# Kernel tuning notes

Measured on AMD Instinct MI355X. Metric: run time of the kernel, lower is better.

## Reference

```python
import jax, jax.numpy as jnp
import numpy as np

B = 16      # batch (num jagged sequences)
N = 1024    # max seq length (mask size n)
D = 512     # embedding_dim
H = 8       # num_heads
DA = 64     # attention_dim per head
DV = 64     # linear_hidden_dim per head
EPS = 1e-6


def setup_inputs() -> dict:
    key = jax.random.key(0)
    k0, k1, k2, k3 = jax.random.split(key, 4)
    lengths = 512 + 16 * np.arange(B)            # deterministic jagged lengths, all <= N
    offsets = np.concatenate([[0], np.cumsum(lengths)]).astype(np.int64)  # (B+1,)
    T = int(offsets[-1])                          # 10112 total tokens
    x = jax.random.normal(k0, (T, D), jnp.float32)
    uvqk = jax.random.normal(k1, (D, 2 * H * DV + 2 * H * DA), jnp.float32) * 0.02
    # torch Linear weight is (out_features, in_features) = (D, H*DV), xavier-uniform scale
    lim = float(np.sqrt(6.0 / (D + H * DV)))
    o_weight = jax.random.uniform(k2, (D, H * DV), jnp.float32, -lim, lim)
    o_bias = jax.random.uniform(k3, (D,), jnp.float32, -0.01, 0.01)
    invalid_attn_mask = jnp.tril(jnp.ones((N, N), jnp.float32))  # causal {0,1} mask
    return {
        "x": x,
        "x_offsets": jnp.asarray(offsets),
        "invalid_attn_mask": invalid_attn_mask,
        "uvqk": uvqk,
        "o_weight": o_weight,
        "o_bias": o_bias,
    }


def _layer_norm(x):
    # F.layer_norm over last dim, no elementwise affine
    m = jnp.mean(x, axis=-1, keepdims=True)
    v = jnp.mean(jnp.square(x - m), axis=-1, keepdims=True)
    return (x - m) / jnp.sqrt(v + EPS)


def _jagged_to_padded(values, offsets, n):
    # values: (T, C) -> (B, n, C), zero padded
    lengths = offsets[1:] - offsets[:-1]               # (B,)
    pos = jnp.arange(n)                                # (n,)
    idx = offsets[:-1, None] + pos[None, :]            # (B, n)
    valid = pos[None, :] < lengths[:, None]            # (B, n)
    idx = jnp.where(valid, idx, 0)
    return values[idx] * valid[..., None].astype(values.dtype)


def _dense_to_jagged(padded, offsets, T):
    # padded: (B, n, C) -> (T, C)
    tok = jnp.arange(T)
    b = jnp.searchsorted(offsets, tok, side="right") - 1   # batch id per token
    p = tok - offsets[b]                                   # position within sequence
    return padded[b, p]


def reference(x, x_offsets, invalid_attn_mask, uvqk, o_weight, o_bias):
    T = x.shape[0]
    n = invalid_attn_mask.shape[-1]
    normed_x = _layer_norm(x)                              # (T, D)
    mm = jax.nn.silu(normed_x @ uvqk)                      # (T, 2*H*DV + 2*H*DA)
    u, v, q, k = jnp.split(mm, [H * DV, 2 * H * DV, 2 * H * DV + H * DA], axis=1)
    pq = _jagged_to_padded(q, x_offsets, n).reshape(-1, n, H, DA)  # (B,n,H,DA)
    pk = _jagged_to_padded(k, x_offsets, n).reshape(-1, n, H, DA)
    pv = _jagged_to_padded(v, x_offsets, n).reshape(-1, n, H, DV)
    qk = jnp.einsum("bqhd,bkhd->bhqk", pq, pk)             # (B,H,n,n)
    qk = (jax.nn.silu(qk) / n) * invalid_attn_mask[None, None]
    attn = jnp.einsum("bhqk,bkhd->bqhd", qk, pv).reshape(-1, n, H * DV)
    attn_j = _dense_to_jagged(attn, x_offsets, T)          # (T, H*DV)
    o_input = u * _layer_norm(attn_j)
    return o_input @ o_weight.T + o_bias + x
```

## Files before the change

kernel.cpp:

```cpp
#include <hip/hip_runtime.h>
#include <hip/hip_bf16.h>
#include <math.h>

typedef short bf16x8 __attribute__((ext_vector_type(8)));
typedef float f32x4 __attribute__((ext_vector_type(4)));

#define MFMA16x16(a, b, c) __builtin_amdgcn_mfma_f32_16x16x32_bf16(a, b, c, 0, 0, 0)

__device__ __forceinline__ float silu_f(float v) { return v / (1.0f + __expf(-v)); }
__device__ __forceinline__ int swz128(int b) { return b ^ (((b >> 7) & 7) << 4); }

__device__ __forceinline__ unsigned short f2bf(float f) {
  union { float f; unsigned u; } x; x.f = f;
  unsigned r = x.u + 0x7fffu + ((x.u >> 16) & 1u);
  return (unsigned short)(r >> 16);
}
__device__ __forceinline__ float bf2f(unsigned short h) {
  union { unsigned u; float f; } x; x.u = ((unsigned)h) << 16;
  return x.f;
}

__device__ __forceinline__ void gload_lds16(const void* g, void* l) {
  __builtin_amdgcn_global_load_lds((__attribute__((address_space(1))) unsigned int*)g,
                                   (__attribute__((address_space(3))) unsigned int*)l,
                                   16, 0, 0);
}

__global__ void k_prep(const int* __restrict__ raw, int Bp1, int* __restrict__ offs,
                       int* __restrict__ tiles, int qtmax) {
  __shared__ int s_off[128], s_nt[128], s_cnt[128], s_base[128];
  int t = threadIdx.x;
  int B = Bp1 - 1;
  bool is64 = (raw[3] == 0);
  if (t < Bp1) { int v = is64 ? raw[2 * t] : raw[t]; offs[t] = v; s_off[t] = v; }
  __syncthreads();
  if (t < B) s_nt[t] = (s_off[t + 1] - s_off[t] + 31) >> 5;
  __syncthreads();
  if (t < qtmax) {
    int c = 0;
    for (int b = 0; b < B; ++b) c += (t < s_nt[b]) ? 1 : 0;
    s_cnt[t] = c;
  }
  __syncthreads();
  if (t < qtmax) {
    int basev = 0;
    for (int q2 = t + 1; q2 < qtmax; ++q2) basev += s_cnt[q2];
    s_base[t] = basev;
  }
  __syncthreads();
  if (t == 0) tiles[0] = (s_base[0] + s_cnt[0]) * 8;
  for (int i = t; i < qtmax * B; i += 256) {
    int qt = i / B, b = i - qt * B;
    if (qt < s_nt[b]) {
      int rank = 0;
      for (int b2 = 0; b2 < b; ++b2) rank += (qt < s_nt[b2]) ? 1 : 0;
      tiles[1 + s_base[qt] + rank] = (b << 16) | qt;
    }
  }
}

__global__ __launch_bounds__(256) void k_conv_uvqkT(const float* __restrict__ uvqk,
                                                    unsigned short* __restrict__ uvqkT) {
  __shared__ float tile[32][33];
  int n0 = blockIdx.x * 32, k0 = blockIdx.y * 32;
  int tx = threadIdx.x & 31;
  int ty = threadIdx.x >> 5;
#pragma unroll
  for (int i = 0; i < 4; ++i)
    tile[ty + 8 * i][tx] = uvqk[(size_t)(k0 + ty + 8 * i) * 2048 + n0 + tx];
  __syncthreads();
#pragma unroll
  for (int i = 0; i < 4; ++i) {
    int nn = ty + 8 * i;
    uvqkT[(size_t)(n0 + nn) * 512 + k0 + tx] = f2bf(tile[tx][nn]);
  }
}

__global__ __launch_bounds__(256) void k_conv_bf16(const float* __restrict__ in,
                                                   unsigned short* __restrict__ out, int n) {
  int i = blockIdx.x * 256 + threadIdx.x;
  if (i < n) out[i] = f2bf(in[i]);
}

__global__ __launch_bounds__(256) void k_ln_x(const float* __restrict__ x,
                                              unsigned short* __restrict__ normed, int T) {
  int lane = threadIdx.x & 63, wid = threadIdx.x >> 6;
  int row = blockIdx.x * 4 + wid;
  if (row >= T) return;
  const float4* xr = (const float4*)(x + (size_t)row * 512);
  float4 a = xr[lane * 2], b = xr[lane * 2 + 1];
  float s = a.x + a.y + a.z + a.w + b.x + b.y + b.z + b.w;
  float s2 = a.x * a.x + a.y * a.y + a.z * a.z + a.w * a.w +
             b.x * b.x + b.y * b.y + b.z * b.z + b.w * b.w;
#pragma unroll
  for (int m = 1; m < 64; m <<= 1) { s += __shfl_xor(s, m); s2 += __shfl_xor(s2, m); }
  float mean = s * (1.0f / 512.0f);
  float var = s2 * (1.0f / 512.0f) - mean * mean;
  float rstd = rsqrtf(var + 1e-6f);
  float v[8] = {a.x, a.y, a.z, a.w, b.x, b.y, b.z, b.w};
  unsigned short o[8];
#pragma unroll
  for (int j = 0; j < 8; ++j) o[j] = f2bf((v[j] - mean) * rstd);
  *(uint4*)(normed + (size_t)row * 512 + lane * 8) = *(uint4*)o;
}

__global__ __launch_bounds__(256) void k_ln_mul_u(const unsigned short* __restrict__ attnb,
                                                  const unsigned short* __restrict__ mm,
                                                  unsigned short* __restrict__ oin, int T) {
  int lane = threadIdx.x & 63, wid = threadIdx.x >> 6;
  int row = blockIdx.x * 4 + wid;
  if (row >= T) return;
  uint4 av = *(const uint4*)(attnb + (size_t)row * 512 + lane * 8);
  const unsigned short* ae = (const unsigned short*)&av;
  float v[8];
#pragma unroll
  for (int j = 0; j < 8; ++j) v[j] = bf2f(ae[j]);
  float s = 0.f, s2 = 0.f;
#pragma unroll
  for (int j = 0; j < 8; ++j) { s += v[j]; s2 += v[j] * v[j]; }
#pragma unroll
  for (int m = 1; m < 64; m <<= 1) { s += __shfl_xor(s, m); s2 += __shfl_xor(s2, m); }
  float mean = s * (1.0f / 512.0f);
  float var = s2 * (1.0f / 512.0f) - mean * mean;
  float rstd = rsqrtf(var + 1e-6f);
  uint4 ub = *(const uint4*)(mm + (size_t)row * 2048 + lane * 8);
  const unsigned short* us = (const unsigned short*)&ub;
  unsigned short o[8];
#pragma unroll
  for (int j = 0; j < 8; ++j) o[j] = f2bf((v[j] - mean) * rstd * bf2f(us[j]));
  *(uint4*)(oin + (size_t)row * 512 + lane * 8) = *(uint4*)o;
}

template <int MODE>
__global__ __launch_bounds__(256) void k_gemm_bt(const unsigned short* __restrict__ A,
                                                 const unsigned short* __restrict__ Bt,
                                                 void* __restrict__ Cout,
                                                 const float* __restrict__ bias,
                                                 const float* __restrict__ xres,
                                                 int M, int Nn, int K, int ntn) {
  __shared__ __align__(16) char lds[32768];
  char* ldsA = lds;
  char* ldsB = lds + 16384;
  int bid = blockIdx.x;
  int mt = bid / ntn, nt = bid - mt * ntn;
  int m0 = mt * 128, n0 = nt * 128;
  int tid = threadIdx.x, lane = tid & 63, wid = tid >> 6;
  int wm = wid >> 1, wn = wid & 1;
  int fr = lane & 15, fq = lane >> 4;
  f32x4 acc[4][4] = {};
  int nK = K >> 6;
  int lco = (lane & 7) * 16;
  int lrow8 = lane >> 3;
  for (int kt = 0; kt < nK; ++kt) {
    int k0 = kt << 6;
#pragma unroll
    for (int p = 0; p < 4; ++p) {
      int chunk = wid * 4 + p;
      int row = chunk * 8 + lrow8;
      int colb = lco ^ ((row & 7) << 4);
      int ar = m0 + row; if (ar >= M) ar = M - 1;
      gload_lds16((const char*)(A + (size_t)ar * K + k0) + colb, ldsA + chunk * 1024);
      gload_lds16((const char*)(Bt + (size_t)(n0 + row) * K + k0) + colb, ldsB + chunk * 1024);
    }
    __syncthreads();
    bf16x8 af[4][2], bfr[4][2];
#pragma unroll
    for (int mi = 0; mi < 4; ++mi) {
      int r = wm * 64 + mi * 16 + fr;
#pragma unroll
      for (int kk = 0; kk < 2; ++kk)
        af[mi][kk] = *(const bf16x8*)(ldsA + swz128(r * 128 + kk * 64 + fq * 16));
    }
#pragma unroll
    for (int ni = 0; ni < 4; ++ni) {
      int r = wn * 64 + ni * 16 + fr;
#pragma unroll
      for (int kk = 0; kk < 2; ++kk)
        bfr[ni][kk] = *(const bf16x8*)(ldsB + swz128(r * 128 + kk * 64 + fq * 16));
    }
#pragma unroll
    for (int mi = 0; mi < 4; ++mi)
#pragma unroll
      for (int ni = 0; ni < 4; ++ni) {
        acc[mi][ni] = MFMA16x16(af[mi][0], bfr[ni][0], acc[mi][ni]);
        acc[mi][ni] = MFMA16x16(af[mi][1], bfr[ni][1], acc[mi][ni]);
      }
    __syncthreads();
  }
#pragma unroll
  for (int mi = 0; mi < 4; ++mi) {
#pragma unroll
    for (int j = 0; j < 4; ++j) {
      int r = m0 + wm * 64 + mi * 16 + fq * 4 + j;
      if (r >= M) continue;
#pragma unroll
      for (int ni = 0; ni < 4; ++ni) {
        int c = n0 + wn * 64 + ni * 16 + fr;
        float v = acc[mi][ni][j];
        if (MODE == 0) {
          ((unsigned short*)Cout)[(size_t)r * Nn + c] = f2bf(silu_f(v));
        } else {
          ((float*)Cout)[(size_t)r * Nn + c] = v + bias[c] + xres[(size_t)r * 512 + c];
        }
      }
    }
  }
}

__global__ __launch_bounds__(256) void k_kv(const unsigned short* __restrict__ mm,
                                            const int* __restrict__ offs,
                                            unsigned short* __restrict__ kC,
                                            unsigned short* __restrict__ vT, int ns) {
  int bh = blockIdx.x; int b = bh >> 3, h = bh & 7;
  int off = offs[b], len = offs[b + 1] - offs[b];
  int tid = threadIdx.x;
  int npad = (len + 63) & ~63;
  const unsigned short* kp = mm + (size_t)off * 2048 + 1536 + h * 64;
  unsigned short* kc = kC + (size_t)bh * ns * 64;
  for (int i = tid; i < npad * 8; i += 256) {
    int row = i >> 3, c8 = (i & 7) * 8;
    uint4 v = {0u, 0u, 0u, 0u};
    if (row < len) v = *(const uint4*)(kp + (size_t)row * 2048 + c8);
    *(uint4*)(kc + row * 64 + c8) = v;
  }
  int lane = tid & 63, w = tid >> 6;
  const unsigned short* vp = mm + (size_t)off * 2048 + 512 + h * 64 + lane;
  unsigned short* vt = vT + ((size_t)bh * 64 + lane) * ns;
  for (int c = w; c < (npad >> 3); c += 4) {
    int s8 = c << 3;
    unsigned short r[8];
#pragma unroll
    for (int j = 0; j < 8; ++j)
      r[j] = (s8 + j < len) ? vp[(size_t)(s8 + j) * 2048] : (unsigned short)0;
    *(uint4*)(vt + s8) = *(uint4*)r;
  }
}

__global__ __launch_bounds__(256) void k_attn3(const unsigned short* __restrict__ mm,
                                               const unsigned short* __restrict__ kC,
                                               const unsigned short* __restrict__ vT,
                                               const int* __restrict__ offs,
                                               const int* __restrict__ tiles,
                                               unsigned short* __restrict__ attnb,
                                               float inv_n, int ns) {
  __shared__ __align__(16) char sP[16384];
  int tid = threadIdx.x, lane = tid & 63, wid = tid >> 6;
  int w = blockIdx.x * 4 + wid;
  if (w >= tiles[0]) return;
  int e = tiles[1 + (w >> 3)];
  int h = w & 7;
  int b = e >> 16, qt = e & 0xffff;
  int bh = b * 8 + h;
  int off = offs[b], len = offs[b + 1] - offs[b];
  int qb = qt * 32;
  int fr = lane & 15, fq = lane >> 4;
  const unsigned short* qp = mm + (size_t)off * 2048 + 1024 + h * 64;
  const unsigned short* kcp = kC + (size_t)bh * ns * 64;
  const unsigned short* vtp = vT + (size_t)bh * 64 * ns;
  bf16x8 aq[2][2];
#pragma unroll
  for (int mi = 0; mi < 2; ++mi) {
    int qr = qb + mi * 16 + fr; if (qr >= len) qr = len - 1;
#pragma unroll
    for (int kk = 0; kk < 2; ++kk)
      aq[mi][kk] = *(const bf16x8*)(qp + (size_t)qr * 2048 + kk * 32 + fq * 8);
  }
  f32x4 accO[2][4] = {};
  char* pw = sP + wid * 4096;
  int nkt = (qb >> 6) + 1;
  for (int kt = 0; kt < nkt; ++kt) {
    int s0 = kt << 6;
    f32x4 sacc[2][4] = {};
#pragma unroll
    for (int ni = 0; ni < 4; ++ni) {
      const unsigned short* kr = kcp + (size_t)(s0 + ni * 16 + fr) * 64 + fq * 8;
      bf16x8 k0 = *(const bf16x8*)kr;
      bf16x8 k1 = *(const bf16x8*)(kr + 32);
#pragma unroll
      for (int mi = 0; mi < 2; ++mi) {
        sacc[mi][ni] = MFMA16x16(aq[mi][0], k0, sacc[mi][ni]);
        sacc[mi][ni] = MFMA16x16(aq[mi][1], k1, sacc[mi][ni]);
      }
    }
    bf16x8 vf[4][2];
#pragma unroll
    for (int nd = 0; nd < 4; ++nd)
#pragma unroll
      for (int kk = 0; kk < 2; ++kk)
        vf[nd][kk] = *(const bf16x8*)(vtp + (size_t)(nd * 16 + fr) * ns + s0 + kk * 32 + fq * 8);
#pragma unroll
    for (int mi = 0; mi < 2; ++mi)
#pragma unroll
      for (int ni = 0; ni < 4; ++ni)
#pragma unroll
        for (int j = 0; j < 4; ++j) {
          int pq = qb + mi * 16 + fq * 4 + j;
          int ps = s0 + ni * 16 + fr;
          float v = (ps <= pq) ? silu_f(sacc[mi][ni][j]) * inv_n : 0.0f;
          *(unsigned short*)(pw + swz128((mi * 16 + fq * 4 + j) * 128 + (ni * 16 + fr) * 2)) =
              f2bf(v);
        }
    bf16x8 pa[2][2];
#pragma unroll
    for (int mi = 0; mi < 2; ++mi) {
      pa[mi][0] = *(const bf16x8*)(pw + swz128((mi * 16 + fr) * 128 + fq * 16));
      pa[mi][1] = *(const bf16x8*)(pw + swz128((mi * 16 + fr) * 128 + 64 + fq * 16));
    }
#pragma unroll
    for (int nd = 0; nd < 4; ++nd)
#pragma unroll
      for (int mi = 0; mi < 2; ++mi) {
        accO[mi][nd] = MFMA16x16(pa[mi][0], vf[nd][0], accO[mi][nd]);
        accO[mi][nd] = MFMA16x16(pa[mi][1], vf[nd][1], accO[mi][nd]);
      }
  }
#pragma unroll
  for (int mi = 0; mi < 2; ++mi)
#pragma unroll
    for (int nd = 0; nd < 4; ++nd)
#pragma unroll
      for (int j = 0; j < 4; ++j) {
        int pq = qb + mi * 16 + fq * 4 + j;
        if (pq < len)
          attnb[(size_t)(off + pq) * 512 + h * 64 + nd * 16 + fr] = f2bf(accO[mi][nd][j]);
      }
}

extern "C" void kernel_launch(void* const* d_in, const int* in_sizes, int n_in,
                              void* d_out, int out_size, void* d_ws, size_t ws_size,
                              hipStream_t stream) {
  const float* x = (const float*)d_in[0];
  const int* xoff = (const int*)d_in[1];
  const float* uvqk = (const float*)d_in[3];
  const float* ow = (const float*)d_in[4];
  const float* obias = (const float*)d_in[5];

  const int D = 512;
  int T = in_sizes[0] / D;
  int B = in_sizes[1] - 1;
  int nm = 1;
  while ((long long)nm * nm < (long long)in_sizes[2]) nm <<= 1;
  int qtmax = nm / 32;

  char* w = (char*)d_ws;
  size_t p = 0;
  auto alloc = [&](size_t bytes) { size_t r = p; p += (bytes + 255) & ~(size_t)255; return r; };
  int* offs = (int*)(w + alloc(sizeof(int) * (size_t)(B + 1)));
  int* tiles = (int*)(w + alloc(sizeof(int) * (size_t)(1 + B * qtmax)));
  unsigned short* normed = (unsigned short*)(w + alloc((size_t)T * 512 * 2));
  unsigned short* mm = (unsigned short*)(w + alloc((size_t)T * 2048 * 2));
  unsigned short* attnb = (unsigned short*)(w + alloc((size_t)T * 512 * 2));
  unsigned short* oin = (unsigned short*)(w + alloc((size_t)T * 512 * 2));
  unsigned short* uvqkT = (unsigned short*)(w + alloc((size_t)2048 * 512 * 2));
  unsigned short* owb = (unsigned short*)(w + alloc((size_t)512 * 512 * 2));
  unsigned short* vT = (unsigned short*)(w + alloc((size_t)B * 8 * 64 * (size_t)nm * 2));
  unsigned short* kC = (unsigned short*)(w + alloc((size_t)B * 8 * (size_t)nm * 64 * 2));

  k_prep<<<1, 256, 0, stream>>>(xoff, B + 1, offs, tiles, qtmax);
  k_conv_uvqkT<<<dim3(64, 16), 256, 0, stream>>>(uvqk, uvqkT);
  k_conv_bf16<<<1024, 256, 0, stream>>>(ow, owb, 512 * 512);
  k_ln_x<<<(T + 3) / 4, 256, 0, stream>>>(x, normed, T);
  int ntm = (T + 127) / 128;
  k_gemm_bt<0><<<ntm * 16, 256, 0, stream>>>(normed, uvqkT, (void*)mm, nullptr, nullptr,
                                             T, 2048, 512, 16);
  k_kv<<<B * 8, 256, 0, stream>>>(mm, offs, kC, vT, nm);
  int maxw = B * qtmax * 8;
  k_attn3<<<(maxw + 3) / 4, 256, 0, stream>>>(mm, kC, vT, offs, tiles, attnb,
                                              1.0f / (float)nm, nm);
  k_ln_mul_u<<<(T + 3) / 4, 256, 0, stream>>>(attnb, mm, oin, T);
  k_gemm_bt<1><<<ntm * 4, 256, 0, stream>>>(oin, owb, d_out, obias, x, T, 512, 512, 4);
}
```

Before: 223.6 us.

## Replace uvqk projection GEMM with 256x256 8-wave ping-pong pipelined kernel

Swaps the 128x128 tile GEMM for the input projection (T x 2048 x 512) with a new 512-thread kernel using 256x256 tiles, double-buffered LDS (128KB), and global->LDS loads split into quarters interleaved with four MFMA phases per K step, with explicit vmcnt waits, raw barriers and s_setprio. The aim is to hide global load latency behind MFMA work and raise per-block data reuse. The cost is heavy LDS use (one block per CU at most, despite launch_bounds asking for 2), many barriers per iteration, and fewer blocks (40x8=320 tiles) for a fairly small GEMM. The epilogue writes scalar bf16 values with silu applied.

Measured after the change: 232.0 us. 1.04x slower.

```diff
diff --git a/kernel.cpp b/kernel.cpp
--- a/kernel.cpp
+++ b/kernel.cpp
@@ -6,6 +6,12 @@
 typedef float f32x4 __attribute__((ext_vector_type(4)));
 
 #define MFMA16x16(a, b, c) __builtin_amdgcn_mfma_f32_16x16x32_bf16(a, b, c, 0, 0, 0)
+#define VMCNT(n) asm volatile("s_waitcnt vmcnt(" #n ")" ::: "memory")
+#define CFENCE asm volatile("" ::: "memory")
+
+__device__ __forceinline__ void barrier_raw() {
+  CFENCE; __builtin_amdgcn_s_barrier(); CFENCE;
+}
 
 __device__ __forceinline__ float silu_f(float v) { return v / (1.0f + __expf(-v)); }
 __device__ __forceinline__ int swz128(int b) { return b ^ (((b >> 7) & 7) << 4); }
@@ -129,6 +135,133 @@
 #pragma unroll
   for (int j = 0; j < 8; ++j) o[j] = f2bf((v[j] - mean) * rstd * bf2f(us[j]));
   *(uint4*)(oin + (size_t)row * 512 + lane * 8) = *(uint4*)o;
+}
+
+__global__ __launch_bounds__(512, 2) void k_gemm8p_silu(
+    const unsigned short* __restrict__ A, const unsigned short* __restrict__ Bt,
+    unsigned short* __restrict__ Cout, int M, int Nn, int K, int ntn) {
+  __shared__ __align__(16) char lds[131072];
+  int bid = blockIdx.x;
+  int mt = bid / ntn, nt = bid - mt * ntn;
+  int m0 = mt * 256, n0 = nt * 256;
+  int tid = threadIdx.x, lane = tid & 63, wid = tid >> 6;
+  int wm = wid >> 2, wn = wid & 3;
+  int fr = lane & 15, fq = lane >> 4;
+  f32x4 acc[8][4] = {};
+  int nK = K >> 6;
+
+  char* const ldsA = lds;
+  char* const ldsB = lds + 65536;
+  int srow = tid >> 3;
+  int scb = ((tid & 7) << 4) ^ ((srow & 7) << 4);
+  int sdst = wid * 1024 + lane * 16;
+
+  auto stageA = [&](char* buf, int kt2, int u) {
+    int row = u * 64 + srow;
+    int ar = m0 + row; if (ar >= M) ar = M - 1;
+    gload_lds16((const char*)(A + (size_t)ar * K + (kt2 << 6)) + scb,
+                buf + u * 8192 + sdst);
+  };
+  auto stageB = [&](char* buf, int kt2, int u) {
+    int row = u * 64 + srow;
+    gload_lds16((const char*)(Bt + (size_t)(n0 + row) * K + (kt2 << 6)) + scb,
+                buf + u * 8192 + sdst);
+  };
+  auto rdA = [&](const char* buf, int mi, int kk) -> bf16x8 {
+    int r = wm * 128 + mi * 16 + fr;
+    return *(const bf16x8*)(buf + swz128(r * 128 + kk * 64 + fq * 16));
+  };
+  auto rdB = [&](const char* buf, int ni, int kk) -> bf16x8 {
+    int r = wn * 64 + ni * 16 + fr;
+    return *(const bf16x8*)(buf + swz128(r * 128 + kk * 64 + fq * 16));
+  };
+
+#pragma unroll
+  for (int u = 0; u < 4; ++u) stageA(ldsA, 0, u);
+#pragma unroll
+  for (int u = 0; u < 4; ++u) stageB(ldsB, 0, u);
+  VMCNT(0);
+  barrier_raw();
+
+  int cur = 0;
+  for (int t = 0; t < nK; ++t) {
+    char* cA = ldsA + cur * 32768;
+    char* cB = ldsB + cur * 32768;
+    char* nA = ldsA + (cur ^ 1) * 32768;
+    char* nB = ldsB + (cur ^ 1) * 32768;
+    bool pf = (t + 1) < nK;
+    bf16x8 a[4][2], b[4][2];
+#pragma unroll
+    for (int mi = 0; mi < 4; ++mi) { a[mi][0] = rdA(cA, mi, 0); a[mi][1] = rdA(cA, mi, 1); }
+#pragma unroll
+    for (int ni = 0; ni < 2; ++ni) { b[ni][0] = rdB(cB, ni, 0); b[ni][1] = rdB(cB, ni, 1); }
+    if (pf) { stageA(nA, t + 1, 0); stageA(nA, t + 1, 2); }
+    barrier_raw();
+    __builtin_amdgcn_s_setprio(1);
+#pragma unroll
+    for (int mi = 0; mi < 4; ++mi)
+#pragma unroll
+      for (int ni = 0; ni < 2; ++ni) {
+        acc[mi][ni] = MFMA16x16(a[mi][0], b[ni][0], acc[mi][ni]);
+        acc[mi][ni] = MFMA16x16(a[mi][1], b[ni][1], acc[mi][ni]);
+      }
+    __builtin_amdgcn_s_setprio(0);
+    barrier_raw();
+#pragma unroll
+    for (int ni = 2; ni < 4; ++ni) { b[ni][0] = rdB(cB, ni, 0); b[ni][1] = rdB(cB, ni, 1); }
+    if (pf) { stageB(nB, t + 1, 0); stageB(nB, t + 1, 1); VMCNT(4); } else { VMCNT(0); }
+    barrier_raw();
+    __builtin_amdgcn_s_setprio(1);
+#pragma unroll
+    for (int mi = 0; mi < 4; ++mi)
+#pragma unroll
+      for (int ni = 2; ni < 4; ++ni) {
+        acc[mi][ni] = MFMA16x16(a[mi][0], b[ni][0], acc[mi][ni]);
+        acc[mi][ni] = MFMA16x16(a[mi][1], b[ni][1], acc[mi][ni]);
+      }
+    __builtin_amdgcn_s_setprio(0);
+    barrier_raw();
+#pragma unroll
+    for (int mi = 0; mi < 4; ++mi) { a[mi][0] = rdA(cA, mi + 4, 0); a[mi][1] = rdA(cA, mi + 4, 1); }
+    if (pf) { stageB(nB, t + 1, 2); stageB(nB, t + 1, 3); }
+    barrier_raw();
+    __builtin_amdgcn_s_setprio(1);
+#pragma unroll
+    for (int mi = 0; mi < 4; ++mi)
+#pragma unroll
+      for (int ni = 0; ni < 2; ++ni) {
+        acc[mi + 4][ni] = MFMA16x16(a[mi][0], b[ni][0], acc[mi + 4][ni]);
+        acc[mi + 4][ni] = MFMA16x16(a[mi][1], b[ni][1], acc[mi + 4][ni]);
+      }
+    __builtin_amdgcn_s_setprio(0);
+    barrier_raw();
+    if (pf) { stageA(nA, t + 1, 1); stageA(nA, t + 1, 3); VMCNT(2); }
+    barrier_raw();
+    __builtin_amdgcn_s_setprio(1);
+#pragma unroll
+    for (int mi = 0; mi < 4; ++mi)
+#pragma unroll
+      for (int ni = 2; ni < 4; ++ni) {
+        acc[mi + 4][ni] = MFMA16x16(a[mi][0], b[ni][0], acc[mi + 4][ni]);
+        acc[mi + 4][ni] = MFMA16x16(a[mi][1], b[ni][1], acc[mi + 4][ni]);
+      }
+    __builtin_amdgcn_s_setprio(0);
+    barrier_raw();
+    cur ^= 1;
+  }
+#pragma unroll
+  for (int mi = 0; mi < 8; ++mi) {
+#pragma unroll
+    for (int j = 0; j < 4; ++j) {
+      int r = m0 + wm * 128 + mi * 16 + fq * 4 + j;
+      if (r >= M) continue;
+#pragma unroll
+      for (int ni = 0; ni < 4; ++ni) {
+        int c = n0 + wn * 64 + ni * 16 + fr;
+        Cout[(size_t)r * Nn + c] = f2bf(silu_f(acc[mi][ni][j]));
+      }
+    }
+  }
 }
 
 template <int MODE>
@@ -360,13 +493,13 @@
   k_conv_uvqkT<<<dim3(64, 16), 256, 0, stream>>>(uvqk, uvqkT);
   k_conv_bf16<<<1024, 256, 0, stream>>>(ow, owb, 512 * 512);
   k_ln_x<<<(T + 3) / 4, 256, 0, stream>>>(x, normed, T);
-  int ntm = (T + 127) / 128;
-  k_gemm_bt<0><<<ntm * 16, 256, 0, stream>>>(normed, uvqkT, (void*)mm, nullptr, nullptr,
-                                             T, 2048, 512, 16);
+  int ntm8 = (T + 255) / 256;
+  k_gemm8p_silu<<<ntm8 * 8, 512, 0, stream>>>(normed, uvqkT, mm, T, 2048, 512, 8);
   k_kv<<<B * 8, 256, 0, stream>>>(mm, offs, kC, vT, nm);
   int maxw = B * qtmax * 8;
   k_attn3<<<(maxw + 3) / 4, 256, 0, stream>>>(mm, kC, vT, offs, tiles, attnb,
                                               1.0f / (float)nm, nm);
   k_ln_mul_u<<<(T + 3) / 4, 256, 0, stream>>>(attnb, mm, oin, T);
+  int ntm = (T + 127) / 128;
   k_gemm_bt<1><<<ntm * 4, 256, 0, stream>>>(oin, owb, d_out, obias, x, T, 512, 512, 4);
 }
```

## Fuse per-head Q/K/V scatter into UVQK GEMM epilogue and use 8-wave GEMM tiles

Applied to the files above, without the earlier changes.

The UVQK GEMM epilogue now writes u, per-head Q and K (row-major padded) and transposed V directly, using a per-token batch/position table built in the prep kernel. This removes the separate k_kv repack pass and the full T x 2048 intermediate buffer. A small zero-fill kernel covers the padded tails. The GEMM also moves to 512 threads with 8 waves each computing a 64x32 sub-tile, and every wave issues its own global-to-LDS loads. The cost is scattered 2-byte stores in the epilogue (V transposed stores are strided), which may hurt write coalescing.

Measured after the change: 233.4 us. +4.4%, slower.

```diff
diff --git a/kernel.cpp b/kernel.cpp
--- a/kernel.cpp
+++ b/kernel.cpp
@@ -27,7 +27,7 @@
 }
 
 __global__ void k_prep(const int* __restrict__ raw, int Bp1, int* __restrict__ offs,
-                       int* __restrict__ tiles, int qtmax) {
+                       int* __restrict__ tiles, int qtmax, int* __restrict__ tok2bp, int T) {
   __shared__ int s_off[128], s_nt[128], s_cnt[128], s_base[128];
   int t = threadIdx.x;
   int B = Bp1 - 1;
@@ -56,6 +56,32 @@
       for (int b2 = 0; b2 < b; ++b2) rank += (qt < s_nt[b2]) ? 1 : 0;
       tiles[1 + s_base[qt] + rank] = (b << 16) | qt;
     }
+  }
+  for (int i = t; i < T; i += 256) {
+    int b = 0;
+    for (int j = 0; j < B; ++j) b += (s_off[j + 1] <= i) ? 1 : 0;
+    tok2bp[i] = (b << 16) | (i - s_off[b]);
+  }
+}
+
+__global__ __launch_bounds__(256) void k_zfill(const int* __restrict__ offs,
+                                               unsigned short* __restrict__ kC,
+                                               unsigned short* __restrict__ vT, int ns) {
+  int bh = blockIdx.x, b = bh >> 3;
+  int len = offs[b + 1] - offs[b];
+  int npad = (len + 63) & ~63;
+  int tail = npad - len;
+  if (tail == 0) return;
+  int tid = threadIdx.x;
+  unsigned short* kc = kC + (size_t)bh * ns * 64 + (size_t)len * 64;
+  for (int i = tid; i < tail * 8; i += 256) {
+    uint4 z = {0u, 0u, 0u, 0u};
+    *(uint4*)(kc + i * 8) = z;
+  }
+  unsigned short* vt = vT + (size_t)bh * 64 * ns;
+  for (int i = tid; i < 64 * tail; i += 256) {
+    int d = i / tail, c = len + (i - d * tail);
+    vt[(size_t)d * ns + c] = 0;
   }
 }
 
@@ -105,7 +131,7 @@
 }
 
 __global__ __launch_bounds__(256) void k_ln_mul_u(const unsigned short* __restrict__ attnb,
-                                                  const unsigned short* __restrict__ mm,
+                                                  const unsigned short* __restrict__ mmu,
                                                   unsigned short* __restrict__ oin, int T) {
   int lane = threadIdx.x & 63, wid = threadIdx.x >> 6;
   int row = blockIdx.x * 4 + wid;
@@ -123,7 +149,7 @@
   float mean = s * (1.0f / 512.0f);
   float var = s2 * (1.0f / 512.0f) - mean * mean;
   float rstd = rsqrtf(var + 1e-6f);
-  uint4 ub = *(const uint4*)(mm + (size_t)row * 2048 + lane * 8);
+  uint4 ub = *(const uint4*)(mmu + (size_t)row * 512 + lane * 8);
   const unsigned short* us = (const unsigned short*)&ub;
   unsigned short o[8];
 #pragma unroll
@@ -132,111 +158,101 @@
 }
 
 template <int MODE>
-__global__ __launch_bounds__(256) void k_gemm_bt(const unsigned short* __restrict__ A,
-                                                 const unsigned short* __restrict__ Bt,
-                                                 void* __restrict__ Cout,
-                                                 const float* __restrict__ bias,
-                                                 const float* __restrict__ xres,
-                                                 int M, int Nn, int K, int ntn) {
+__global__ __launch_bounds__(512, 4) void k_gemm8w(
+    const unsigned short* __restrict__ A, const unsigned short* __restrict__ Bt,
+    int M, int K, int Nn, int ntn,
+    unsigned short* __restrict__ mmu, unsigned short* __restrict__ qC,
+    unsigned short* __restrict__ kC, unsigned short* __restrict__ vT,
+    const int* __restrict__ tok2bp, int ns,
+    float* __restrict__ Cout, const float* __restrict__ bias, const float* __restrict__ xres) {
   __shared__ __align__(16) char lds[32768];
-  char* ldsA = lds;
-  char* ldsB = lds + 16384;
+  char* const ldsA = lds;
+  char* const ldsB = lds + 16384;
   int bid = blockIdx.x;
   int mt = bid / ntn, nt = bid - mt * ntn;
   int m0 = mt * 128, n0 = nt * 128;
   int tid = threadIdx.x, lane = tid & 63, wid = tid >> 6;
-  int wm = wid >> 1, wn = wid & 1;
+  int wm = wid >> 2, wn = wid & 3;
   int fr = lane & 15, fq = lane >> 4;
-  f32x4 acc[4][4] = {};
+  f32x4 acc[4][2] = {};
   int nK = K >> 6;
-  int lco = (lane & 7) * 16;
-  int lrow8 = lane >> 3;
+  int srow = wid * 16 + (lane >> 3);
+  int scb = (((lane & 7) ^ (lane >> 3)) << 4);
+  char* const dstA0 = ldsA + wid * 2048;
+  char* const dstA1 = ldsA + wid * 2048 + 1024;
+  char* const dstB0 = ldsB + wid * 2048;
+  char* const dstB1 = ldsB + wid * 2048 + 1024;
+  int ar0 = m0 + srow; if (ar0 >= M) ar0 = M - 1;
+  int ar1 = m0 + srow + 8; if (ar1 >= M) ar1 = M - 1;
+  const char* gA0 = (const char*)(A + (size_t)ar0 * K) + scb;
+  const char* gA1 = (const char*)(A + (size_t)ar1 * K) + scb;
+  const char* gB0 = (const char*)(Bt + (size_t)(n0 + srow) * K) + scb;
+  const char* gB1 = (const char*)(Bt + (size_t)(n0 + srow + 8) * K) + scb;
+
   for (int kt = 0; kt < nK; ++kt) {
-    int k0 = kt << 6;
-#pragma unroll
-    for (int p = 0; p < 4; ++p) {
-      int chunk = wid * 4 + p;
-      int row = chunk * 8 + lrow8;
-      int colb = lco ^ ((row & 7) << 4);
-      int ar = m0 + row; if (ar >= M) ar = M - 1;
-      gload_lds16((const char*)(A + (size_t)ar * K + k0) + colb, ldsA + chunk * 1024);
-      gload_lds16((const char*)(Bt + (size_t)(n0 + row) * K + k0) + colb, ldsB + chunk * 1024);
-    }
+    gload_lds16(gA0 + (kt << 7), dstA0);
+    gload_lds16(gA1 + (kt << 7), dstA1);
+    gload_lds16(gB0 + (kt << 7), dstB0);
+    gload_lds16(gB1 + (kt << 7), dstB1);
     __syncthreads();
-    bf16x8 af[4][2], bfr[4][2];
+    bf16x8 a[4][2], b[2][2];
 #pragma unroll
     for (int mi = 0; mi < 4; ++mi) {
       int r = wm * 64 + mi * 16 + fr;
 #pragma unroll
       for (int kk = 0; kk < 2; ++kk)
-        af[mi][kk] = *(const bf16x8*)(ldsA + swz128(r * 128 + kk * 64 + fq * 16));
-    }
-#pragma unroll
-    for (int ni = 0; ni < 4; ++ni) {
-      int r = wn * 64 + ni * 16 + fr;
+        a[mi][kk] = *(const bf16x8*)(ldsA + swz128(r * 128 + kk * 64 + fq * 16));
+    }
+#pragma unroll
+    for (int ni = 0; ni < 2; ++ni) {
+      int r = wn * 32 + ni * 16 + fr;
 #pragma unroll
       for (int kk = 0; kk < 2; ++kk)
-        bfr[ni][kk] = *(const bf16x8*)(ldsB + swz128(r * 128 + kk * 64 + fq * 16));
+        b[ni][kk] = *(const bf16x8*)(ldsB + swz128(r * 128 + kk * 64 + fq * 16));
     }
 #pragma unroll
     for (int mi = 0; mi < 4; ++mi)
 #pragma unroll
-      for (int ni = 0; ni < 4; ++ni) {
-        acc[mi][ni] = MFMA16x16(af[mi][0], bfr[ni][0], acc[mi][ni]);
-        acc[mi][ni] = MFMA16x16(af[mi][1], bfr[ni][1], acc[mi][ni]);
+      for (int ni = 0; ni < 2; ++ni) {
+        acc[mi][ni] = MFMA16x16(a[mi][0], b[ni][0], acc[mi][ni]);
+        acc[mi][ni] = MFMA16x16(a[mi][1], b[ni][1], acc[mi][ni]);
       }
     __syncthreads();
   }
+  int c0 = n0 + wn * 32;
 #pragma unroll
   for (int mi = 0; mi < 4; ++mi) {
 #pragma unroll
     for (int j = 0; j < 4; ++j) {
       int r = m0 + wm * 64 + mi * 16 + fq * 4 + j;
       if (r >= M) continue;
-#pragma unroll
-      for (int ni = 0; ni < 4; ++ni) {
-        int c = n0 + wn * 64 + ni * 16 + fr;
-        float v = acc[mi][ni][j];
-        if (MODE == 0) {
-          ((unsigned short*)Cout)[(size_t)r * Nn + c] = f2bf(silu_f(v));
-        } else {
-          ((float*)Cout)[(size_t)r * Nn + c] = v + bias[c] + xres[(size_t)r * 512 + c];
+      if (MODE == 0) {
+        int bp = tok2bp[r];
+        int bb = bp >> 16, pos = bp & 0xffff;
+#pragma unroll
+        for (int ni = 0; ni < 2; ++ni) {
+          int c = c0 + ni * 16 + fr;
+          unsigned short bf = f2bf(silu_f(acc[mi][ni][j]));
+          int reg = c >> 9;
+          int h = (c >> 6) & 7, d = c & 63;
+          size_t bh = (size_t)(bb * 8 + h);
+          if (reg == 0) mmu[(size_t)r * 512 + c] = bf;
+          else if (reg == 1) vT[(bh * 64 + d) * ns + pos] = bf;
+          else if (reg == 2) qC[(bh * ns + pos) * 64 + d] = bf;
+          else kC[(bh * ns + pos) * 64 + d] = bf;
         }
-      }
-    }
-  }
-}
-
-__global__ __launch_bounds__(256) void k_kv(const unsigned short* __restrict__ mm,
-                                            const int* __restrict__ offs,
-                                            unsigned short* __restrict__ kC,
-                                            unsigned short* __restrict__ vT, int ns) {
-  int bh = blockIdx.x; int b = bh >> 3, h = bh & 7;
-  int off = offs[b], len = offs[b + 1] - offs[b];
-  int tid = threadIdx.x;
-  int npad = (len + 63) & ~63;
-  const unsigned short* kp = mm + (size_t)off * 2048 + 1536 + h * 64;
-  unsigned short* kc = kC + (size_t)bh * ns * 64;
-  for (int i = tid; i < npad * 8; i += 256) {
-    int row = i >> 3, c8 = (i & 7) * 8;
-    uint4 v = {0u, 0u, 0u, 0u};
-    if (row < len) v = *(const uint4*)(kp + (size_t)row * 2048 + c8);
-    *(uint4*)(kc + row * 64 + c8) = v;
-  }
-  int lane = tid & 63, w = tid >> 6;
-  const unsigned short* vp = mm + (size_t)off * 2048 + 512 + h * 64 + lane;
-  unsigned short* vt = vT + ((size_t)bh * 64 + lane) * ns;
-  for (int c = w; c < (npad >> 3); c += 4) {
-    int s8 = c << 3;
-    unsigned short r[8];
-#pragma unroll
-    for (int j = 0; j < 8; ++j)
-      r[j] = (s8 + j < len) ? vp[(size_t)(s8 + j) * 2048] : (unsigned short)0;
-    *(uint4*)(vt + s8) = *(uint4*)r;
-  }
-}
-
-__global__ __launch_bounds__(256) void k_attn3(const unsigned short* __restrict__ mm,
+      } else {
+#pragma unroll
+        for (int ni = 0; ni < 2; ++ni) {
+          int c = c0 + ni * 16 + fr;
+          Cout[(size_t)r * Nn + c] = acc[mi][ni][j] + bias[c] + xres[(size_t)r * 512 + c];
+        }
+      }
+    }
+  }
+}
+
+__global__ __launch_bounds__(256) void k_attn3(const unsigned short* __restrict__ qC,
                                                const unsigned short* __restrict__ kC,
                                                const unsigned short* __restrict__ vT,
                                                const int* __restrict__ offs,
@@ -254,7 +270,7 @@
   int off = offs[b], len = offs[b + 1] - offs[b];
   int qb = qt * 32;
   int fr = lane & 15, fq = lane >> 4;
-  const unsigned short* qp = mm + (size_t)off * 2048 + 1024 + h * 64;
+  const unsigned short* qp = qC + (size_t)bh * ns * 64;
   const unsigned short* kcp = kC + (size_t)bh * ns * 64;
   const unsigned short* vtp = vT + (size_t)bh * 64 * ns;
   bf16x8 aq[2][2];
@@ -263,7 +279,7 @@
     int qr = qb + mi * 16 + fr; if (qr >= len) qr = len - 1;
 #pragma unroll
     for (int kk = 0; kk < 2; ++kk)
-      aq[mi][kk] = *(const bf16x8*)(qp + (size_t)qr * 2048 + kk * 32 + fq * 8);
+      aq[mi][kk] = *(const bf16x8*)(qp + (size_t)qr * 64 + kk * 32 + fq * 8);
   }
   f32x4 accO[2][4] = {};
   char* pw = sP + wid * 4096;
@@ -347,26 +363,31 @@
   auto alloc = [&](size_t bytes) { size_t r = p; p += (bytes + 255) & ~(size_t)255; return r; };
   int* offs = (int*)(w + alloc(sizeof(int) * (size_t)(B + 1)));
   int* tiles = (int*)(w + alloc(sizeof(int) * (size_t)(1 + B * qtmax)));
+  int* tok2bp = (int*)(w + alloc(sizeof(int) * (size_t)T));
   unsigned short* normed = (unsigned short*)(w + alloc((size_t)T * 512 * 2));
-  unsigned short* mm = (unsigned short*)(w + alloc((size_t)T * 2048 * 2));
+  unsigned short* mmu = (unsigned short*)(w + alloc((size_t)T * 512 * 2));
   unsigned short* attnb = (unsigned short*)(w + alloc((size_t)T * 512 * 2));
   unsigned short* oin = (unsigned short*)(w + alloc((size_t)T * 512 * 2));
   unsigned short* uvqkT = (unsigned short*)(w + alloc((size_t)2048 * 512 * 2));
   unsigned short* owb = (unsigned short*)(w + alloc((size_t)512 * 512 * 2));
+  unsigned short* qC = (unsigned short*)(w + alloc((size_t)B * 8 * (size_t)nm * 64 * 2));
+  unsigned short* kC = (unsigned short*)(w + alloc((size_t)B * 8 * (size_t)nm * 64 * 2));
   unsigned short* vT = (unsigned short*)(w + alloc((size_t)B * 8 * 64 * (size_t)nm * 2));
-  unsigned short* kC = (unsigned short*)(w + alloc((size_t)B * 8 * (size_t)nm * 64 * 2));
-
-  k_prep<<<1, 256, 0, stream>>>(xoff, B + 1, offs, tiles, qtmax);
+
+  k_prep<<<1, 256, 0, stream>>>(xoff, B + 1, offs, tiles, qtmax, tok2bp, T);
+  k_zfill<<<B * 8, 256, 0, stream>>>(offs, kC, vT, nm);
   k_conv_uvqkT<<<dim3(64, 16), 256, 0, stream>>>(uvqk, uvqkT);
   k_conv_bf16<<<1024, 256, 0, stream>>>(ow, owb, 512 * 512);
   k_ln_x<<<(T + 3) / 4, 256, 0, stream>>>(x, normed, T);
   int ntm = (T + 127) / 128;
-  k_gemm_bt<0><<<ntm * 16, 256, 0, stream>>>(normed, uvqkT, (void*)mm, nullptr, nullptr,
-                                             T, 2048, 512, 16);
-  k_kv<<<B * 8, 256, 0, stream>>>(mm, offs, kC, vT, nm);
+  k_gemm8w<0><<<ntm * 16, 512, 0, stream>>>(normed, uvqkT, T, 512, 2048, 16,
+                                            mmu, qC, kC, vT, tok2bp, nm,
+                                            nullptr, nullptr, nullptr);
   int maxw = B * qtmax * 8;
-  k_attn3<<<(maxw + 3) / 4, 256, 0, stream>>>(mm, kC, vT, offs, tiles, attnb,
+  k_attn3<<<(maxw + 3) / 4, 256, 0, stream>>>(qC, kC, vT, offs, tiles, attnb,
                                               1.0f / (float)nm, nm);
-  k_ln_mul_u<<<(T + 3) / 4, 256, 0, stream>>>(attnb, mm, oin, T);
-  k_gemm_bt<1><<<ntm * 4, 256, 0, stream>>>(oin, owb, d_out, obias, x, T, 512, 512, 4);
-}
+  k_ln_mul_u<<<(T + 3) / 4, 256, 0, stream>>>(attnb, mmu, oin, T);
+  k_gemm8w<1><<<ntm * 4, 512, 0, stream>>>(oin, owb, T, 512, 512, 4,
+                                           nullptr, nullptr, nullptr, nullptr, nullptr, nm,
+                                           (float*)d_out, obias, x);
+}
```
